# Optimization experiments

Measured on AMD Instinct MI355X. Metric: run time of the kernel, lower is better.

The kernel has to match this reference:

```python
import jax, jax.numpy as jnp
import numpy as np

N = 32768      # total nodes = 256 graphs x 128 nodes
G = 256        # graphs in batch
NPG = 128      # nodes per graph
DEG = 8        # incoming edges per node
E = N * DEG    # 262144 edges
F_IN = 64      # node feature size
F_E = 16       # edge feature size
EMB = 64       # out_channels per head == embedding_size
H = 4          # attention heads
HC = H * EMB   # 256
DENSE = 256
K = 64         # ceil(0.5 * NPG)
EPS = 1e-5


def setup_inputs() -> dict:
    key = jax.random.key(0)
    ks = list(jax.random.split(key, 32))
    it = iter(ks)
    s = 0.05

    def rn(shape):
        return jax.random.normal(next(it), shape, jnp.float32) * s

    x = jax.random.normal(next(it), (N, F_IN), jnp.float32)
    dst = jnp.repeat(jnp.arange(N, dtype=jnp.int32), DEG)
    src = (dst // NPG) * NPG + jax.random.randint(next(it), (E,), 0, NPG, dtype=jnp.int32)
    edge_index = jnp.stack([src, dst])                      # [2, E], edges stay within graph
    edge_attr = jax.random.normal(next(it), (E, F_E), jnp.float32)
    batch_index = jnp.arange(N, dtype=jnp.int32) // NPG

    inp = dict(
        x=x, edge_index=edge_index, edge_attr=edge_attr, batch_index=batch_index,
        # TransformerConv 1 (in=F_IN)
        Wq1=rn((F_IN, HC)), bq1=jnp.zeros((HC,), jnp.float32),
        Wk1=rn((F_IN, HC)), bk1=jnp.zeros((HC,), jnp.float32),
        Wv1=rn((F_IN, HC)), bv1=jnp.zeros((HC,), jnp.float32),
        We1=rn((F_E, HC)),
        Ws1=rn((F_IN, HC)), bs1=jnp.zeros((HC,), jnp.float32),
        Wb1=rn((3 * HC, 1)),
        t1_W=rn((HC, EMB)), t1_b=jnp.zeros((EMB,), jnp.float32),
        bn1_g=jnp.ones((EMB,), jnp.float32), bn1_b=jnp.zeros((EMB,), jnp.float32),
        # TransformerConv 2 (in=EMB)
        Wq2=rn((EMB, HC)), bq2=jnp.zeros((HC,), jnp.float32),
        Wk2=rn((EMB, HC)), bk2=jnp.zeros((HC,), jnp.float32),
        Wv2=rn((EMB, HC)), bv2=jnp.zeros((HC,), jnp.float32),
        We2=rn((F_E, HC)),
        Ws2=rn((EMB, HC)), bs2=jnp.zeros((HC,), jnp.float32),
        Wb2=rn((3 * HC, 1)),
        t2_W=rn((HC, EMB)), t2_b=jnp.zeros((EMB,), jnp.float32),
        bn2_g=jnp.ones((EMB,), jnp.float32), bn2_b=jnp.zeros((EMB,), jnp.float32),
        # TopKPooling + MLP head
        pool_w=rn((EMB,)),
        l1_W=rn((2 * EMB, DENSE)), l1_b=jnp.zeros((DENSE,), jnp.float32),
        l2_W=rn((DENSE, DENSE // 2)), l2_b=jnp.zeros((DENSE // 2,), jnp.float32),
        l3_W=rn((DENSE // 2, 1)), l3_b=jnp.zeros((1,), jnp.float32),
    )
    return inp


def _tconv(x, src, dst, ea, Wq, bq, Wk, bk, Wv, bv, We, Ws, bs, Wb):
    """PyG TransformerConv with edge_dim, beta=True, concat=True."""
    n = x.shape[0]
    q = (x @ Wq + bq).reshape(n, H, EMB)                    # [N,H,C]
    eemb = (ea @ We).reshape(-1, H, EMB)                    # [E,H,C]
    k = (x @ Wk + bk)[src].reshape(-1, H, EMB) + eemb       # edge features added to key
    v = (x @ Wv + bv)[src].reshape(-1, H, EMB) + eemb       # and to value
    alpha = jnp.einsum('ehc,ehc->eh', q[dst], k) / jnp.sqrt(jnp.float32(EMB))  # [E,H]
    # stable segment softmax over incoming edges of each dst node
    amax = jax.ops.segment_max(alpha, dst, num_segments=n)
    pexp = jnp.exp(alpha - amax[dst])
    denom = jax.ops.segment_sum(pexp, dst, num_segments=n)
    attn = pexp / denom[dst]                                # [E,H]
    out = jax.ops.segment_sum(v * attn[..., None], dst, num_segments=n).reshape(n, HC)
    # beta gated skip: lin_skip(x) and lin_beta([out, xr, out-xr])
    xr = x @ Ws + bs
    beta = jax.nn.sigmoid(jnp.concatenate([out, xr, out - xr], axis=-1) @ Wb)  # [N,1]
    return beta * xr + (1.0 - beta) * out


def _bn(x, g, b):
    m = x.mean(0)
    v = x.var(0)
    return g * (x - m) * jax.lax.rsqrt(v + EPS) + b


def _forward(x, edge_attr,
             Wq1, bq1, Wk1, bk1, Wv1, bv1, We1, Ws1, bs1, Wb1, t1_W, t1_b, bn1_g, bn1_b,
             Wq2, bq2, Wk2, bk2, Wv2, bv2, We2, Ws2, bs2, Wb2, t2_W, t2_b, bn2_g, bn2_b,
             pool_w, l1_W, l1_b, l2_W, l2_b, l3_W, l3_b,
             edge_index, batch_index):
    src, dst = edge_index[0], edge_index[1]
    h = _tconv(x, src, dst, edge_attr, Wq1, bq1, Wk1, bk1, Wv1, bv1, We1, Ws1, bs1, Wb1)
    h = _bn(jax.nn.relu(h @ t1_W + t1_b), bn1_g, bn1_b)
    h = _tconv(h, src, dst, edge_attr, Wq2, bq2, Wk2, bk2, Wv2, bv2, We2, Ws2, bs2, Wb2)
    h = _bn(jax.nn.relu(h @ t2_W + t2_b), bn2_g, bn2_b)
    # TopKPooling: score = (x.w)/||w||, keep top K per graph, scale by tanh(score)
    score = (h @ pool_w) / jnp.linalg.norm(pool_w)          # [N]
    sv, si = jax.lax.top_k(score.reshape(G, NPG), K)        # [G,K]
    xs = jnp.take_along_axis(h.reshape(G, NPG, EMB), si[..., None], axis=1)  # [G,K,EMB]
    xs = xs * jnp.tanh(sv)[..., None]
    # readout: global max pool || global mean pool
    rep = jnp.concatenate([xs.max(axis=1), xs.mean(axis=1)], axis=-1)  # [G, 2*EMB]
    hd = jax.nn.relu(rep @ l1_W + l1_b)
    hd = jax.nn.relu(hd @ l2_W + l2_b)
    return hd @ l3_W + l3_b                                  # [G,1]


def reference(x, edge_index, edge_attr, batch_index,
              Wq1, bq1, Wk1, bk1, Wv1, bv1, We1, Ws1, bs1, Wb1, t1_W, t1_b, bn1_g, bn1_b,
              Wq2, bq2, Wk2, bk2, Wv2, bv2, We2, Ws2, bs2, Wb2, t2_W, t2_b, bn2_g, bn2_b,
              pool_w, l1_W, l1_b, l2_W, l2_b, l3_W, l3_b):
    return _forward(x, edge_attr,
                    Wq1, bq1, Wk1, bk1, Wv1, bv1, We1, Ws1, bs1, Wb1, t1_W, t1_b, bn1_g, bn1_b,
                    Wq2, bq2, Wk2, bk2, Wv2, bv2, We2, Ws2, bs2, Wb2, t2_W, t2_b, bn2_g, bn2_b,
                    pool_w, l1_W, l1_b, l2_W, l2_b, l3_W, l3_b,
                    edge_index, batch_index)
```

## Files before the change

kernel.cpp:

```cpp
#include <hip/hip_runtime.h>
#include <math.h>

#define NN 32768
#define NG 256
#define DEG 8
#define HC 256
#define NCAT 1088
#define HCP 320
#define KTOP 64
#define EPSBN 1e-5f

typedef __attribute__((ext_vector_type(8))) short short8v;
typedef __attribute__((ext_vector_type(4))) float f32x4;

__device__ inline float bf2f(unsigned short u) {
    union { unsigned int i; float f; } c; c.i = ((unsigned int)u) << 16; return c.f;
}
__device__ inline unsigned short f2bf(float f) {
    union { float f; unsigned int i; } c; c.f = f;
    unsigned int r = c.i + 0x7FFFu + ((c.i >> 16) & 1u);
    return (unsigned short)(r >> 16);
}
__device__ inline void split2(float v, unsigned short& hi, unsigned short& lo) {
    hi = f2bf(v);
    union { float f; unsigned int i; } c; c.f = v - bf2f(hi);
    lo = (unsigned short)(c.i >> 16);
}
__device__ inline int permcol(int n) {
    if (n < 256 || n >= 768) return n;
    if (n < 512) { int l = n - 256; return 256 + ((l >> 2) << 3) + (l & 3); }
    int l = n - 512; return 256 + ((l >> 2) << 3) + 4 + (l & 3);
}

__device__ void prep_dev(int b, int t,
    const float* __restrict__ Wq, const float* __restrict__ bq,
    const float* __restrict__ Wk, const float* __restrict__ bk,
    const float* __restrict__ Wv, const float* __restrict__ bv,
    const float* __restrict__ Ws, const float* __restrict__ bs,
    const float* __restrict__ We, const float* __restrict__ tW,
    const float* __restrict__ Wb,
    unsigned short* __restrict__ WThi, unsigned short* __restrict__ WTlo,
    float* __restrict__ bcat,
    unsigned short* __restrict__ tWThi, unsigned short* __restrict__ tWTlo,
    float* __restrict__ Wbf, float* __restrict__ stats)
{
    if (b < 16) {
        int n = b * 64 + (t >> 2);
        int cc = n & 255;
        const float* src = (n < 256) ? Wq : (n < 512) ? Wk : (n < 768) ? Wv : Ws;
        int p = permcol(n);
        int k0 = (t & 3) * 16;
        #pragma unroll
        for (int k = k0; k < k0 + 16; k++) {
            unsigned short h, l;
            split2(src[k * 256 + cc], h, l);
            WThi[p * 64 + k] = h; WTlo[p * 64 + k] = l;
        }
    } else if (b < 32) {
        int idx = (b - 16) * 256 + t;
        int k = idx >> 6, o = idx & 63;
        int h = o >> 4, f = o & 15;
        const float* wq = Wq + k * 256 + h * 64;
        const float* we = We + f * 256 + h * 64;
        float s = 0.f;
        #pragma unroll
        for (int d = 0; d < 64; d++) s += wq[d] * we[d];
        unsigned short hh, ll;
        split2(s, hh, ll);
        WThi[(1024 + o) * 64 + k] = hh; WTlo[(1024 + o) * 64 + k] = ll;
    } else if (b < 48) {
        int idx = (b - 32) * 256 + t;
        int kp = idx >> 6, n = idx & 63;
        int h = kp >> 4, f = kp & 15;
        const float* we = We + f * 256 + h * 64;
        const float* tw = tW + (h * 64) * 64 + n;
        float s = 0.f;
        #pragma unroll
        for (int d = 0; d < 64; d++) s += we[d] * tw[d * 64];
        unsigned short hh, ll;
        split2(s, hh, ll);
        tWThi[n * HCP + 256 + kp] = hh; tWTlo[n * HCP + 256 + kp] = ll;
    } else if (b < 64) {
        int base = (b - 48) * 1024 + t * 4;
        #pragma unroll
        for (int i = 0; i < 4; i++) {
            int idx = base + i;
            int n = idx >> 8, k = idx & 255;
            unsigned short h, l;
            split2(tW[k * 64 + n], h, l);
            tWThi[n * HCP + k] = h; tWTlo[n * HCP + k] = l;
        }
    } else {
        if (t < 128) stats[t] = 0.f;
        Wbf[t]       = Wb[t]       + Wb[512 + t];
        Wbf[256 + t] = Wb[256 + t] - Wb[512 + t];
        for (int c = t; c < 1024; c += 256) {
            int cc = c & 255;
            float v = (c < 256) ? bq[cc] : (c < 512) ? bk[cc] : (c < 768) ? bv[cc] : bs[cc];
            bcat[permcol(c)] = v;
        }
        if (t < 64) {
            int h = t >> 4, f = t & 15;
            const float* we = We + f * 256 + h * 64;
            float s = 0.f, sb = 0.f;
            #pragma unroll
            for (int d = 0; d < 64; d++) {
                s  += we[d] * (Wb[h * 64 + d] + Wb[512 + h * 64 + d]);
                sb += we[d] * bq[h * 64 + d];
            }
            Wbf[512 + t] = s;
            bcat[1024 + t] = sb;
        }
    }
}

__global__ __launch_bounds__(256) void prep_all(
    const float* Wq1, const float* bq1, const float* Wk1, const float* bk1,
    const float* Wv1, const float* bv1, const float* Ws1, const float* bs1,
    const float* We1, const float* t1W, const float* Wb1,
    unsigned short* WThi1, unsigned short* WTlo1, float* bcat1,
    unsigned short* tWThi1, unsigned short* tWTlo1, float* Wbf1, float* stats1,
    const float* Wq2, const float* bq2, const float* Wk2, const float* bk2,
    const float* Wv2, const float* bv2, const float* Ws2, const float* bs2,
    const float* We2, const float* t2W, const float* Wb2,
    unsigned short* WThi2, unsigned short* WTlo2, float* bcat2,
    unsigned short* tWThi2, unsigned short* tWTlo2, float* Wbf2, float* stats2)
{
    const int b = blockIdx.x, t = threadIdx.x;
    if (b < 65)
        prep_dev(b, t, Wq1, bq1, Wk1, bk1, Wv1, bv1, Ws1, bs1, We1, t1W, Wb1,
                 WThi1, WTlo1, bcat1, tWThi1, tWTlo1, Wbf1, stats1);
    else
        prep_dev(b - 65, t, Wq2, bq2, Wk2, bk2, Wv2, bv2, Ws2, bs2, We2, t2W, Wb2,
                 WThi2, WTlo2, bcat2, tWThi2, tWTlo2, Wbf2, stats2);
}

__global__ __launch_bounds__(256) void proj_mfma(
    const float* __restrict__ A, const float* __restrict__ stats,
    const float* __restrict__ gbn, const float* __restrict__ bbn,
    const unsigned short* __restrict__ WThi, const unsigned short* __restrict__ WTlo,
    const float* __restrict__ bcat, unsigned short* __restrict__ C)
{
    __shared__ char smem[32768];
    unsigned short* AhiL = (unsigned short*)smem;
    unsigned short* AloL = AhiL + 4096;
    unsigned short* WhiL = AloL + 4096;
    unsigned short* WloL = WhiL + 4096;
    float* CL = (float*)smem;
    __shared__ float scl[64], sft[64];
    const int t = threadIdx.x;
    const int n0 = blockIdx.x * 64;
    const int row0 = blockIdx.y * 64;
    const int w = t >> 6, l = t & 63;
    const int lr = l & 15, lg = l >> 4, ls = l & 7;

    if (t < 64) {
        if (stats) {
            float mean = stats[t] * (1.f / NN);
            float var  = stats[64 + t] * (1.f / NN) - mean * mean;
            float s = gbn[t] * rsqrtf(var + EPSBN);
            scl[t] = s; sft[t] = bbn[t] - mean * s;
        } else { scl[t] = 1.f; sft[t] = 0.f; }
    }
    __syncthreads();

    #pragma unroll
    for (int g = 0; g < 2; g++) {
        int idx = t * 8 + g * 2048;
        int r = idx >> 6, c = idx & 63;
        int ch = (c >> 3) ^ (r & 7);
        float4 a0 = *(const float4*)(A + (size_t)(row0 + r) * 64 + c);
        float4 a1 = *(const float4*)(A + (size_t)(row0 + r) * 64 + c + 4);
        float av[8] = {a0.x, a0.y, a0.z, a0.w, a1.x, a1.y, a1.z, a1.w};
        short8v vh, vl;
        #pragma unroll
        for (int j = 0; j < 8; j++) {
            float v = av[j] * scl[c + j] + sft[c + j];
            unsigned short h2, l2;
            split2(v, h2, l2);
            vh[j] = (short)h2; vl[j] = (short)l2;
        }
        *(short8v*)(AhiL + r * 64 + ch * 8) = vh;
        *(short8v*)(AloL + r * 64 + ch * 8) = vl;
        *(short8v*)(WhiL + r * 64 + ch * 8) =
            *(const short8v*)(WThi + (size_t)(n0 + r) * 64 + c);
        *(short8v*)(WloL + r * 64 + ch * 8) =
            *(const short8v*)(WTlo + (size_t)(n0 + r) * 64 + c);
    }
    __syncthreads();

    f32x4 acc[4] = {};
    #pragma unroll
    for (int kk = 0; kk < 2; kk++) {
        int ch = (kk * 4 + lg) ^ ls;
        short8v ah = *(short8v*)(AhiL + (w * 16 + lr) * 64 + ch * 8);
        short8v al = *(short8v*)(AloL + (w * 16 + lr) * 64 + ch * 8);
        #pragma unroll
        for (int nt = 0; nt < 4; nt++) {
            short8v bh = *(short8v*)(WhiL + (nt * 16 + lr) * 64 + ch * 8);
            short8v bl = *(short8v*)(WloL + (nt * 16 + lr) * 64 + ch * 8);
            acc[nt] = __builtin_amdgcn_mfma_f32_16x16x32_bf16(ah, bh, acc[nt], 0, 0, 0);
            acc[nt] = __builtin_amdgcn_mfma_f32_16x16x32_bf16(al, bh, acc[nt], 0, 0, 0);
            acc[nt] = __builtin_amdgcn_mfma_f32_16x16x32_bf16(ah, bl, acc[nt], 0, 0, 0);
        }
    }
    __syncthreads();
    #pragma unroll
    for (int nt = 0; nt < 4; nt++)
        #pragma unroll
        for (int r = 0; r < 4; r++)
            CL[(w * 16 + lg * 4 + r) * 68 + nt * 16 + lr] = acc[nt][r];
    __syncthreads();
    {
        int r = t >> 2, cb = (t & 3) * 16;
        #pragma unroll
        for (int jj = 0; jj < 2; jj++) {
            f32x4 p0 = *(f32x4*)(CL + r * 68 + cb + jj * 8);
            f32x4 p1 = *(f32x4*)(CL + r * 68 + cb + jj * 8 + 4);
            float4 b0 = *(const float4*)(bcat + n0 + cb + jj * 8);
            float4 b1 = *(const float4*)(bcat + n0 + cb + jj * 8 + 4);
            short8v o;
            o[0] = (short)f2bf(p0[0] + b0.x); o[1] = (short)f2bf(p0[1] + b0.y);
            o[2] = (short)f2bf(p0[2] + b0.z); o[3] = (short)f2bf(p0[3] + b0.w);
            o[4] = (short)f2bf(p1[0] + b1.x); o[5] = (short)f2bf(p1[1] + b1.y);
            o[6] = (short)f2bf(p1[2] + b1.z); o[7] = (short)f2bf(p1[3] + b1.w);
            *(short8v*)(C + (size_t)(row0 + r) * NCAT + n0 + cb + jj * 8) = o;
        }
    }
}

__global__ __launch_bounds__(256) void gemm_t(
    const unsigned short* __restrict__ Ahi, const unsigned short* __restrict__ Alo,
    const unsigned short* __restrict__ WThi, const unsigned short* __restrict__ WTlo,
    const float* __restrict__ bias, float* __restrict__ Tout,
    float* __restrict__ stats)
{
    __shared__ char smem[32768];
    unsigned short* AhiL = (unsigned short*)smem;
    unsigned short* AloL = AhiL + 4096;
    unsigned short* WhiL = AloL + 4096;
    unsigned short* WloL = WhiL + 4096;
    float* CL = (float*)smem;
    const int t = threadIdx.x;
    const int row0 = blockIdx.x * 64;
    const int w = t >> 6, l = t & 63;
    const int lr = l & 15, lg = l >> 4, ls = l & 7;
    f32x4 acc[4] = {};
    for (int kt = 0; kt < 5; kt++) {
        if (kt) __syncthreads();
        #pragma unroll
        for (int g = 0; g < 2; g++) {
            int idx = t * 8 + g * 2048;
            int r = idx >> 6, c = idx & 63;
            int ch = (c >> 3) ^ (r & 7);
            *(short8v*)(AhiL + r * 64 + ch * 8) =
                *(const short8v*)(Ahi + (size_t)(row0 + r) * HCP + kt * 64 + c);
            *(short8v*)(AloL + r * 64 + ch * 8) =
                *(const short8v*)(Alo + (size_t)(row0 + r) * HCP + kt * 64 + c);
            *(short8v*)(WhiL + r * 64 + ch * 8) =
                *(const short8v*)(WThi + r * HCP + kt * 64 + c);
            *(short8v*)(WloL + r * 64 + ch * 8) =
                *(const short8v*)(WTlo + r * HCP + kt * 64 + c);
        }
        __syncthreads();
        #pragma unroll
        for (int kk = 0; kk < 2; kk++) {
            int ch = (kk * 4 + lg) ^ ls;
            short8v ah = *(short8v*)(AhiL + (w * 16 + lr) * 64 + ch * 8);
            short8v al = *(short8v*)(AloL + (w * 16 + lr) * 64 + ch * 8);
            #pragma unroll
            for (int nt = 0; nt < 4; nt++) {
                short8v bh = *(short8v*)(WhiL + (nt * 16 + lr) * 64 + ch * 8);
                short8v bl = *(short8v*)(WloL + (nt * 16 + lr) * 64 + ch * 8);
                acc[nt] = __builtin_amdgcn_mfma_f32_16x16x32_bf16(ah, bh, acc[nt], 0, 0, 0);
                acc[nt] = __builtin_amdgcn_mfma_f32_16x16x32_bf16(al, bh, acc[nt], 0, 0, 0);
                acc[nt] = __builtin_amdgcn_mfma_f32_16x16x32_bf16(ah, bl, acc[nt], 0, 0, 0);
            }
        }
    }
    __syncthreads();
    #pragma unroll
    for (int nt = 0; nt < 4; nt++)
        #pragma unroll
        for (int r = 0; r < 4; r++)
            CL[(w * 16 + lg * 4 + r) * 68 + nt * 16 + lr] = acc[nt][r];
    __syncthreads();
    {
        int r = t >> 2, cb = (t & 3) * 16;
        #pragma unroll
        for (int jj = 0; jj < 4; jj++) {
            f32x4 p = *(f32x4*)(CL + r * 68 + cb + jj * 4);
            float4 bb = *(const float4*)(bias + cb + jj * 4);
            float4 o;
            o.x = fmaxf(p[0] + bb.x, 0.f); o.y = fmaxf(p[1] + bb.y, 0.f);
            o.z = fmaxf(p[2] + bb.z, 0.f); o.w = fmaxf(p[3] + bb.w, 0.f);
            *(float4*)(Tout + (size_t)(row0 + r) * 64 + cb + jj * 4) = o;
        }
    }
    if (t < 64) {
        float bb = bias[t];
        float s = 0.f, s2 = 0.f;
        #pragma unroll 8
        for (int r = 0; r < 64; r++) {
            float v = fmaxf(CL[r * 68 + t] + bb, 0.f);
            s += v; s2 += v * v;
        }
        atomicAdd(&stats[t], s);
        atomicAdd(&stats[64 + t], s2);
    }
}

__global__ __launch_bounds__(256, 6) void attn_fused(
    const unsigned short* __restrict__ C,
    const float* __restrict__ Wbf,
    const int* __restrict__ srcIdx, const float* __restrict__ EA,
    unsigned short* __restrict__ Hhi, unsigned short* __restrict__ Hlo)
{
    const int t = threadIdx.x;
    const int lane = t & 63;
    const int wave = t >> 6;
    const int bid = blockIdx.x;
    const int swz = (bid & 7) * 1024 + (bid >> 3);
    const int n = swz * 4 + wave;
    const int c0 = lane * 4;
    const int h = lane >> 4;
    const int fi = lane & 15;

    const unsigned short* rowN = C + (size_t)n * NCAT;
    ushort4 qv = *(const ushort4*)(rowN + c0);
    float q0 = bf2f(qv.x), q1 = bf2f(qv.y), q2 = bf2f(qv.z), q3 = bf2f(qv.w);
    float qe_l = bf2f(rowN[1024 + h * 16 + fi]);

    const int ebase = n * DEG;
    int sj = srcIdx[ebase + (lane & 7)];
    int ss[DEG];
    #pragma unroll
    for (int j = 0; j < DEG; j++) ss[j] = __shfl(sj, j);

    short8v kv[DEG];
    float eav[DEG];
    #pragma unroll
    for (int j = 0; j < DEG; j++) {
        kv[j] = *(const short8v*)(C + (size_t)ss[j] * NCAT + 256 + lane * 8);
        eav[j] = EA[(size_t)(ebase + j) * 16 + fi];
    }
    float alpha[DEG];
    #pragma unroll
    for (int j = 0; j < DEG; j++) {
        float d = eav[j] * qe_l
                + q0 * bf2f((unsigned short)kv[j][0]) + q1 * bf2f((unsigned short)kv[j][1])
                + q2 * bf2f((unsigned short)kv[j][2]) + q3 * bf2f((unsigned short)kv[j][3]);
        d += __shfl_xor(d, 1); d += __shfl_xor(d, 2);
        d += __shfl_xor(d, 4); d += __shfl_xor(d, 8);
        alpha[j] = d * 0.125f;
    }
    float mx = alpha[0];
    #pragma unroll
    for (int j = 1; j < DEG; j++) mx = fmaxf(mx, alpha[j]);
    float wsum = 0.f;
    #pragma unroll
    for (int j = 0; j < DEG; j++) { alpha[j] = __expf(alpha[j] - mx); wsum += alpha[j]; }
    float inv = __builtin_amdgcn_rcpf(wsum);

    float o0 = 0.f, o1 = 0.f, o2 = 0.f, o3 = 0.f, eg = 0.f;
    #pragma unroll
    for (int j = 0; j < DEG; j++) {
        float wj = alpha[j] * inv;
        eg += wj * eav[j];
        o0 += wj * bf2f((unsigned short)kv[j][4]);
        o1 += wj * bf2f((unsigned short)kv[j][5]);
        o2 += wj * bf2f((unsigned short)kv[j][6]);
        o3 += wj * bf2f((unsigned short)kv[j][7]);
    }

    ushort4 sv = *(const ushort4*)(rowN + 768 + c0);
    float xr0 = bf2f(sv.x), xr1 = bf2f(sv.y), xr2 = bf2f(sv.z), xr3 = bf2f(sv.w);

    float part = eg * Wbf[512 + lane];
    {
        f32x4 w13 = *(const f32x4*)(Wbf + c0);
        f32x4 w23 = *(const f32x4*)(Wbf + 256 + c0);
        part += o0 * w13[0] + o1 * w13[1] + o2 * w13[2] + o3 * w13[3];
        part += xr0 * w23[0] + xr1 * w23[1] + xr2 * w23[2] + xr3 * w23[3];
    }
    part += __shfl_xor(part, 1);  part += __shfl_xor(part, 2);
    part += __shfl_xor(part, 4);  part += __shfl_xor(part, 8);
    part += __shfl_xor(part, 16); part += __shfl_xor(part, 32);
    float beta = __builtin_amdgcn_rcpf(1.f + __expf(-part));
    float omb = 1.f - beta;

    ushort4 hh, hl;
    split2(beta * xr0 + omb * o0, hh.x, hl.x);
    split2(beta * xr1 + omb * o1, hh.y, hl.y);
    split2(beta * xr2 + omb * o2, hh.z, hl.z);
    split2(beta * xr3 + omb * o3, hh.w, hl.w);
    *(ushort4*)(Hhi + (size_t)n * HCP + c0) = hh;
    *(ushort4*)(Hlo + (size_t)n * HCP + c0) = hl;

    unsigned short zh, zl;
    split2(omb * eg, zh, zl);
    Hhi[(size_t)n * HCP + 256 + lane] = zh;
    Hlo[(size_t)n * HCP + 256 + lane] = zl;
}

__global__ __launch_bounds__(128) void pool_mlp(
    const float* __restrict__ Hn, const float* __restrict__ stats,
    const float* __restrict__ gbn, const float* __restrict__ bbn,
    const float* __restrict__ pw,
    const float* __restrict__ W1, const float* __restrict__ b1,
    const float* __restrict__ W2, const float* __restrict__ b2,
    const float* __restrict__ W3, const float* __restrict__ b3,
    float* __restrict__ out)
{
    __shared__ float sh[128][65];
    __shared__ float spw[64];
    __shared__ float sc[128];
    __shared__ float sscale[128];
    __shared__ int   skeep[128];
    __shared__ float rmax[2][64], rsum[2][64];
    __shared__ float srep[128];
    __shared__ float sh1[256];
    __shared__ float sh2[128];
    __shared__ float wred[2];
    __shared__ float scl[64], sft[64];
    const int g = blockIdx.x, t = threadIdx.x;

    if (t < 64) {
        float mean = stats[t] * (1.f / NN);
        float var  = stats[64 + t] * (1.f / NN) - mean * mean;
        float s = gbn[t] * rsqrtf(var + EPSBN);
        scl[t] = s; sft[t] = bbn[t] - mean * s;
        spw[t] = pw[t];
    }
    __syncthreads();
    for (int i = t; i < 128 * 64; i += 128) {
        int c = i & 63;
        sh[i >> 6][c] = Hn[(size_t)g * 128 * 64 + i] * scl[c] + sft[c];
    }
    __syncthreads();

    float nw = 0.f;
    #pragma unroll
    for (int i = 0; i < 64; i++) { float w = spw[i]; nw += w * w; }
    float invn = rsqrtf(nw);

    float s = 0.f;
    #pragma unroll
    for (int i = 0; i < 64; i++) s += sh[t][i] * spw[i];
    s *= invn;
    sc[t] = s;
    __syncthreads();

    int rank = 0;
    for (int m = 0; m < 128; m++) {
        float sm = sc[m];
        rank += (sm > s) || (sm == s && m < t);
    }
    skeep[t] = (rank < KTOP);
    sscale[t] = tanhf(s);
    __syncthreads();

    {
        int c = t & 63, half = t >> 6;
        float mxv = -1e30f, sm = 0.f;
        for (int r = half * 64; r < half * 64 + 64; r++) {
            if (skeep[r]) {
                float v = sh[r][c] * sscale[r];
                mxv = fmaxf(mxv, v); sm += v;
            }
        }
        rmax[half][c] = mxv; rsum[half][c] = sm;
    }
    __syncthreads();
    if (t < 64) {
        srep[t] = fmaxf(rmax[0][t], rmax[1][t]);
        srep[64 + t] = (rsum[0][t] + rsum[1][t]) * (1.f / KTOP);
    }
    __syncthreads();

    #pragma unroll
    for (int jj = 0; jj < 2; jj++) {
        int j = t + jj * 128;
        float a = b1[j];
        for (int c2 = 0; c2 < 128; c2++) a += srep[c2] * W1[c2 * 256 + j];
        sh1[j] = fmaxf(a, 0.f);
    }
    __syncthreads();
    {
        float a = b2[t];
        for (int c2 = 0; c2 < 256; c2++) a += sh1[c2] * W2[c2 * 128 + t];
        sh2[t] = fmaxf(a, 0.f);
    }
    __syncthreads();
    float p = sh2[t] * W3[t];
    p += __shfl_xor(p, 1);  p += __shfl_xor(p, 2);  p += __shfl_xor(p, 4);
    p += __shfl_xor(p, 8);  p += __shfl_xor(p, 16); p += __shfl_xor(p, 32);
    if ((t & 63) == 0) wred[t >> 6] = p;
    __syncthreads();
    if (t == 0) out[g] = wred[0] + wred[1] + b3[0];
}

extern "C" void kernel_launch(void* const* d_in, const int* in_sizes, int n_in,
                              void* d_out, int out_size, void* d_ws, size_t ws_size,
                              hipStream_t stream)
{
    const float* x    = (const float*)d_in[0];
    const int*   ei   = (const int*)  d_in[1];
    const float* ea   = (const float*)d_in[2];
    const int*   srcI = ei;
    const float* Wq1 = (const float*)d_in[4];  const float* bq1 = (const float*)d_in[5];
    const float* Wk1 = (const float*)d_in[6];  const float* bk1 = (const float*)d_in[7];
    const float* Wv1 = (const float*)d_in[8];  const float* bv1 = (const float*)d_in[9];
    const float* We1 = (const float*)d_in[10];
    const float* Ws1 = (const float*)d_in[11]; const float* bs1 = (const float*)d_in[12];
    const float* Wb1 = (const float*)d_in[13];
    const float* t1W = (const float*)d_in[14]; const float* t1b = (const float*)d_in[15];
    const float* g1  = (const float*)d_in[16]; const float* be1 = (const float*)d_in[17];
    const float* Wq2 = (const float*)d_in[18]; const float* bq2 = (const float*)d_in[19];
    const float* Wk2 = (const float*)d_in[20]; const float* bk2 = (const float*)d_in[21];
    const float* Wv2 = (const float*)d_in[22]; const float* bv2 = (const float*)d_in[23];
    const float* We2 = (const float*)d_in[24];
    const float* Ws2 = (const float*)d_in[25]; const float* bs2 = (const float*)d_in[26];
    const float* Wb2 = (const float*)d_in[27];
    const float* t2W = (const float*)d_in[28]; const float* t2b = (const float*)d_in[29];
    const float* g2  = (const float*)d_in[30]; const float* be2 = (const float*)d_in[31];
    const float* pw  = (const float*)d_in[32];
    const float* l1W = (const float*)d_in[33]; const float* l1b = (const float*)d_in[34];
    const float* l2W = (const float*)d_in[35]; const float* l2b = (const float*)d_in[36];
    const float* l3W = (const float*)d_in[37]; const float* l3b = (const float*)d_in[38];

    char* ws = (char*)d_ws;
    unsigned short* C   = (unsigned short*)ws;
    unsigned short* Hhi = (unsigned short*)(ws + (size_t)NN * NCAT * 2);
    unsigned short* Hlo = Hhi + (size_t)NN * HCP;
    float* bT   = (float*)(Hlo + (size_t)NN * HCP);
    float* bT2  = bT + (size_t)NN * 64;
    float* bcat1  = bT2 + (size_t)NN * 64;
    float* bcat2  = bcat1 + NCAT;
    float* stats1 = bcat2 + NCAT;
    float* stats2 = stats1 + 128;
    float* Wbf1   = stats2 + 128;
    float* Wbf2   = Wbf1 + 576;
    unsigned short* WThi1  = (unsigned short*)(Wbf2 + 576);
    unsigned short* WTlo1  = WThi1 + (size_t)NCAT * 64;
    unsigned short* WThi2  = WTlo1 + (size_t)NCAT * 64;
    unsigned short* WTlo2  = WThi2 + (size_t)NCAT * 64;
    unsigned short* tWThi1 = WTlo2 + (size_t)NCAT * 64;
    unsigned short* tWTlo1 = tWThi1 + 64 * HCP;
    unsigned short* tWThi2 = tWTlo1 + 64 * HCP;
    unsigned short* tWTlo2 = tWThi2 + 64 * HCP;

    const dim3 blk(256);
    const dim3 gProj(17, 512);

    prep_all<<<130, blk, 0, stream>>>(
        Wq1, bq1, Wk1, bk1, Wv1, bv1, Ws1, bs1, We1, t1W, Wb1,
        WThi1, WTlo1, bcat1, tWThi1, tWTlo1, Wbf1, stats1,
        Wq2, bq2, Wk2, bk2, Wv2, bv2, Ws2, bs2, We2, t2W, Wb2,
        WThi2, WTlo2, bcat2, tWThi2, tWTlo2, Wbf2, stats2);

    proj_mfma<<<gProj, blk, 0, stream>>>(x, nullptr, nullptr, nullptr,
                                         WThi1, WTlo1, bcat1, C);
    attn_fused<<<NN / 4, blk, 0, stream>>>(C, Wbf1, srcI, ea, Hhi, Hlo);
    gemm_t<<<512, blk, 0, stream>>>(Hhi, Hlo, tWThi1, tWTlo1, t1b, bT, stats1);

    proj_mfma<<<gProj, blk, 0, stream>>>(bT, stats1, g1, be1,
                                         WThi2, WTlo2, bcat2, C);
    attn_fused<<<NN / 4, blk, 0, stream>>>(C, Wbf2, srcI, ea, Hhi, Hlo);
    gemm_t<<<512, blk, 0, stream>>>(Hhi, Hlo, tWThi2, tWTlo2, t2b, bT2, stats2);

    pool_mlp<<<NG, 128, 0, stream>>>(bT2, stats2, g2, be2, pw,
                                     l1W, l1b, l2W, l2b, l3W, l3b,
                                     (float*)d_out);
}
```

Baseline: 193.7 us.

## Split BN+bf16 split into separate kernel; load MFMA operands directly from global

Adds a split_bn kernel that applies batch-norm scaling and writes hi/lo bf16 copies of the activations to a workspace. proj_mfma is recomputed 17 times per row block, so it no longer redoes the BN and split work on every call. Both proj_mfma and gemm_t now read MFMA fragments straight from global memory instead of staging through swizzled LDS, which removes those barriers. The cost is an extra kernel launch, an extra round trip of the activations through memory, and fragment loads that depend on L1/L2 hits rather than LDS reuse.

```diff
diff --git a/kernel.cpp b/kernel.cpp
--- a/kernel.cpp
+++ b/kernel.cpp
@@ -135,25 +135,13 @@
                  WThi2, WTlo2, bcat2, tWThi2, tWTlo2, Wbf2, stats2);
 }
 
-__global__ __launch_bounds__(256) void proj_mfma(
+__global__ __launch_bounds__(256) void split_bn(
     const float* __restrict__ A, const float* __restrict__ stats,
     const float* __restrict__ gbn, const float* __restrict__ bbn,
-    const unsigned short* __restrict__ WThi, const unsigned short* __restrict__ WTlo,
-    const float* __restrict__ bcat, unsigned short* __restrict__ C)
-{
-    __shared__ char smem[32768];
-    unsigned short* AhiL = (unsigned short*)smem;
-    unsigned short* AloL = AhiL + 4096;
-    unsigned short* WhiL = AloL + 4096;
-    unsigned short* WloL = WhiL + 4096;
-    float* CL = (float*)smem;
+    unsigned short* __restrict__ Xhi, unsigned short* __restrict__ Xlo)
+{
     __shared__ float scl[64], sft[64];
     const int t = threadIdx.x;
-    const int n0 = blockIdx.x * 64;
-    const int row0 = blockIdx.y * 64;
-    const int w = t >> 6, l = t & 63;
-    const int lr = l & 15, lg = l >> 4, ls = l & 7;
-
     if (t < 64) {
         if (stats) {
             float mean = stats[t] * (1.f / NN);
@@ -163,48 +151,51 @@
         } else { scl[t] = 1.f; sft[t] = 0.f; }
     }
     __syncthreads();
-
-    #pragma unroll
-    for (int g = 0; g < 2; g++) {
-        int idx = t * 8 + g * 2048;
-        int r = idx >> 6, c = idx & 63;
-        int ch = (c >> 3) ^ (r & 7);
-        float4 a0 = *(const float4*)(A + (size_t)(row0 + r) * 64 + c);
-        float4 a1 = *(const float4*)(A + (size_t)(row0 + r) * 64 + c + 4);
-        float av[8] = {a0.x, a0.y, a0.z, a0.w, a1.x, a1.y, a1.z, a1.w};
-        short8v vh, vl;
-        #pragma unroll
-        for (int j = 0; j < 8; j++) {
-            float v = av[j] * scl[c + j] + sft[c + j];
-            unsigned short h2, l2;
-            split2(v, h2, l2);
-            vh[j] = (short)h2; vl[j] = (short)l2;
-        }
-        *(short8v*)(AhiL + r * 64 + ch * 8) = vh;
-        *(short8v*)(AloL + r * 64 + ch * 8) = vl;
-        *(short8v*)(WhiL + r * 64 + ch * 8) =
-            *(const short8v*)(WThi + (size_t)(n0 + r) * 64 + c);
-        *(short8v*)(WloL + r * 64 + ch * 8) =
-            *(const short8v*)(WTlo + (size_t)(n0 + r) * 64 + c);
-    }
-    __syncthreads();
+    size_t i8 = ((size_t)blockIdx.x * 256 + t) * 8;
+    int c0 = (int)(i8 & 63);
+    float4 a0 = *(const float4*)(A + i8);
+    float4 a1 = *(const float4*)(A + i8 + 4);
+    float av[8] = {a0.x, a0.y, a0.z, a0.w, a1.x, a1.y, a1.z, a1.w};
+    short8v vh, vl;
+    #pragma unroll
+    for (int j = 0; j < 8; j++) {
+        float v = av[j] * scl[c0 + j] + sft[c0 + j];
+        unsigned short h, l;
+        split2(v, h, l);
+        vh[j] = (short)h; vl[j] = (short)l;
+    }
+    *(short8v*)(Xhi + i8) = vh;
+    *(short8v*)(Xlo + i8) = vl;
+}
+
+__global__ __launch_bounds__(256) void proj_mfma(
+    const unsigned short* __restrict__ Ahi, const unsigned short* __restrict__ Alo,
+    const unsigned short* __restrict__ WThi, const unsigned short* __restrict__ WTlo,
+    const float* __restrict__ bcat, unsigned short* __restrict__ C)
+{
+    __shared__ float CL[64 * 68];
+    const int t = threadIdx.x;
+    const int n0 = blockIdx.x * 64;
+    const int row0 = blockIdx.y * 64;
+    const int w = t >> 6, l = t & 63;
+    const int lr = l & 15, lg = l >> 4;
 
     f32x4 acc[4] = {};
     #pragma unroll
     for (int kk = 0; kk < 2; kk++) {
-        int ch = (kk * 4 + lg) ^ ls;
-        short8v ah = *(short8v*)(AhiL + (w * 16 + lr) * 64 + ch * 8);
-        short8v al = *(short8v*)(AloL + (w * 16 + lr) * 64 + ch * 8);
+        size_t aoff = (size_t)(row0 + w * 16 + lr) * 64 + (kk * 4 + lg) * 8;
+        short8v ah = *(const short8v*)(Ahi + aoff);
+        short8v al = *(const short8v*)(Alo + aoff);
         #pragma unroll
         for (int nt = 0; nt < 4; nt++) {
-            short8v bh = *(short8v*)(WhiL + (nt * 16 + lr) * 64 + ch * 8);
-            short8v bl = *(short8v*)(WloL + (nt * 16 + lr) * 64 + ch * 8);
+            size_t woff = (size_t)(n0 + nt * 16 + lr) * 64 + (kk * 4 + lg) * 8;
+            short8v bh = *(const short8v*)(WThi + woff);
+            short8v bl = *(const short8v*)(WTlo + woff);
             acc[nt] = __builtin_amdgcn_mfma_f32_16x16x32_bf16(ah, bh, acc[nt], 0, 0, 0);
             acc[nt] = __builtin_amdgcn_mfma_f32_16x16x32_bf16(al, bh, acc[nt], 0, 0, 0);
             acc[nt] = __builtin_amdgcn_mfma_f32_16x16x32_bf16(ah, bl, acc[nt], 0, 0, 0);
         }
     }
-    __syncthreads();
     #pragma unroll
     for (int nt = 0; nt < 4; nt++)
         #pragma unroll
@@ -235,50 +226,29 @@
     const float* __restrict__ bias, float* __restrict__ Tout,
     float* __restrict__ stats)
 {
-    __shared__ char smem[32768];
-    unsigned short* AhiL = (unsigned short*)smem;
-    unsigned short* AloL = AhiL + 4096;
-    unsigned short* WhiL = AloL + 4096;
-    unsigned short* WloL = WhiL + 4096;
-    float* CL = (float*)smem;
+    __shared__ float CL[64 * 68];
     const int t = threadIdx.x;
     const int row0 = blockIdx.x * 64;
     const int w = t >> 6, l = t & 63;
-    const int lr = l & 15, lg = l >> 4, ls = l & 7;
+    const int lr = l & 15, lg = l >> 4;
     f32x4 acc[4] = {};
     for (int kt = 0; kt < 5; kt++) {
-        if (kt) __syncthreads();
-        #pragma unroll
-        for (int g = 0; g < 2; g++) {
-            int idx = t * 8 + g * 2048;
-            int r = idx >> 6, c = idx & 63;
-            int ch = (c >> 3) ^ (r & 7);
-            *(short8v*)(AhiL + r * 64 + ch * 8) =
-                *(const short8v*)(Ahi + (size_t)(row0 + r) * HCP + kt * 64 + c);
-            *(short8v*)(AloL + r * 64 + ch * 8) =
-                *(const short8v*)(Alo + (size_t)(row0 + r) * HCP + kt * 64 + c);
-            *(short8v*)(WhiL + r * 64 + ch * 8) =
-                *(const short8v*)(WThi + r * HCP + kt * 64 + c);
-            *(short8v*)(WloL + r * 64 + ch * 8) =
-                *(const short8v*)(WTlo + r * HCP + kt * 64 + c);
-        }
-        __syncthreads();
         #pragma unroll
         for (int kk = 0; kk < 2; kk++) {
-            int ch = (kk * 4 + lg) ^ ls;
-            short8v ah = *(short8v*)(AhiL + (w * 16 + lr) * 64 + ch * 8);
-            short8v al = *(short8v*)(AloL + (w * 16 + lr) * 64 + ch * 8);
+            size_t aoff = (size_t)(row0 + w * 16 + lr) * HCP + kt * 64 + (kk * 4 + lg) * 8;
+            short8v ah = *(const short8v*)(Ahi + aoff);
+            short8v al = *(const short8v*)(Alo + aoff);
             #pragma unroll
             for (int nt = 0; nt < 4; nt++) {
-                short8v bh = *(short8v*)(WhiL + (nt * 16 + lr) * 64 + ch * 8);
-                short8v bl = *(short8v*)(WloL + (nt * 16 + lr) * 64 + ch * 8);
+                size_t woff = (size_t)(nt * 16 + lr) * HCP + kt * 64 + (kk * 4 + lg) * 8;
+                short8v bh = *(const short8v*)(WThi + woff);
+                short8v bl = *(const short8v*)(WTlo + woff);
                 acc[nt] = __builtin_amdgcn_mfma_f32_16x16x32_bf16(ah, bh, acc[nt], 0, 0, 0);
                 acc[nt] = __builtin_amdgcn_mfma_f32_16x16x32_bf16(al, bh, acc[nt], 0, 0, 0);
                 acc[nt] = __builtin_amdgcn_mfma_f32_16x16x32_bf16(ah, bl, acc[nt], 0, 0, 0);
             }
         }
     }
-    __syncthreads();
     #pragma unroll
     for (int nt = 0; nt < 4; nt++)
         #pragma unroll
@@ -535,7 +505,9 @@
     unsigned short* Hlo = Hhi + (size_t)NN * HCP;
     float* bT   = (float*)(Hlo + (size_t)NN * HCP);
     float* bT2  = bT + (size_t)NN * 64;
-    float* bcat1  = bT2 + (size_t)NN * 64;
+    unsigned short* Xhi = (unsigned short*)(bT2 + (size_t)NN * 64);
+    unsigned short* Xlo = Xhi + (size_t)NN * 64;
+    float* bcat1  = (float*)(Xlo + (size_t)NN * 64);
     float* bcat2  = bcat1 + NCAT;
     float* stats1 = bcat2 + NCAT;
     float* stats2 = stats1 + 128;
@@ -559,13 +531,15 @@
         Wq2, bq2, Wk2, bk2, Wv2, bv2, Ws2, bs2, We2, t2W, Wb2,
         WThi2, WTlo2, bcat2, tWThi2, tWTlo2, Wbf2, stats2);
 
-    proj_mfma<<<gProj, blk, 0, stream>>>(x, nullptr, nullptr, nullptr,
-                                         WThi1, WTlo1, bcat1, C);
+    split_bn<<<NN * 64 / (256 * 8), blk, 0, stream>>>(x, nullptr, nullptr, nullptr,
+                                                      Xhi, Xlo);
+    proj_mfma<<<gProj, blk, 0, stream>>>(Xhi, Xlo, WThi1, WTlo1, bcat1, C);
     attn_fused<<<NN / 4, blk, 0, stream>>>(C, Wbf1, srcI, ea, Hhi, Hlo);
     gemm_t<<<512, blk, 0, stream>>>(Hhi, Hlo, tWThi1, tWTlo1, t1b, bT, stats1);
 
-    proj_mfma<<<gProj, blk, 0, stream>>>(bT, stats1, g1, be1,
-                                         WThi2, WTlo2, bcat2, C);
+    split_bn<<<NN * 64 / (256 * 8), blk, 0, stream>>>(bT, stats1, g1, be1,
+                                                      Xhi, Xlo);
+    proj_mfma<<<gProj, blk, 0, stream>>>(Xhi, Xlo, WThi2, WTlo2, bcat2, C);
     attn_fused<<<NN / 4, blk, 0, stream>>>(C, Wbf2, srcI, ea, Hhi, Hlo);
     gemm_t<<<512, blk, 0, stream>>>(Hhi, Hlo, tWThi2, tWTlo2, t2b, bT2, stats2);
 
```

After: 346.1 us. 1.79x slower.
